# Kernel tuning notes

Measured on AMD Instinct MI355X. Metric: run time of the kernel, lower is better.

Reference implementation:

```python
import jax, jax.numpy as jnp
import numpy as np


def setup_inputs() -> dict:
    key = jax.random.key(0)
    k1, k2 = jax.random.split(key)
    B, C, H = 1024, 1000, 512  # batch, classes, hidden
    y = jax.random.normal(k1, (B, C), dtype=jnp.float32)
    w = jax.random.normal(k2, (C, H), dtype=jnp.float32)
    epsilon = jnp.ones((), dtype=jnp.float32)
    lipschitz = jnp.ones((), dtype=jnp.float32)
    return {"y": y, "w": w, "epsilon": epsilon, "lipschitz": lipschitz}


def reference(y, w, epsilon, lipschitz):
    # y: [B, C] logits; w: [C, H] final-layer weight
    kW = lipschitz * w.T                      # [H, C]
    j = jnp.argmax(y, axis=1)                 # [B]
    y_j = jnp.max(y, axis=1, keepdims=True)   # [B, 1]
    kW_j = kW.T[j]                            # [B, H] gather of argmax column
    kW_ij = kW_j[:, :, None] - kW[None]       # [B, H, C] broadcast difference
    sq = jnp.sum(kW_ij * kW_ij, axis=1)       # [B, C]
    # safe sqrt (value identical; avoids NaN grad at the exact-zero j column)
    K_ij = jnp.where(sq > 0, jnp.sqrt(jnp.where(sq > 0, sq, 1.0)), 0.0)
    y_bot_i = y + epsilon * K_ij              # [B, C]
    y_bot_i = jnp.where(y == y_j, -jnp.inf, y_bot_i)
    y_bot = jnp.max(y_bot_i, axis=1, keepdims=True)  # [B, 1]
    return jnp.concatenate([y, y_bot], axis=1)       # [B, C+1]
```

## Files before the change

### kernel.cpp

```cpp
#include <hip/hip_runtime.h>
#include <math.h>

#define B_SZ 1024
#define C_SZ 1000
#define H_SZ 512


typedef __attribute__((ext_vector_type(8))) short bf16x8;
typedef __attribute__((ext_vector_type(4))) float f32x4;

#define KC 128
#define RS 136

__device__ __forceinline__ uint4 pack8(float4 a, float4 b) {
    unsigned e[8] = {__float_as_uint(a.x), __float_as_uint(a.y),
                     __float_as_uint(a.z), __float_as_uint(a.w),
                     __float_as_uint(b.x), __float_as_uint(b.y),
                     __float_as_uint(b.z), __float_as_uint(b.w)};
    unsigned short h[8];
#pragma unroll
    for (int i = 0; i < 8; ++i) {
        unsigned v = e[i];
        v += 0x7fffu + ((v >> 16) & 1u);
        h[i] = (unsigned short)(v >> 16);
    }
    uint4 p;
    p.x = (unsigned)h[0] | ((unsigned)h[1] << 16);
    p.y = (unsigned)h[2] | ((unsigned)h[3] << 16);
    p.z = (unsigned)h[4] | ((unsigned)h[5] << 16);
    p.w = (unsigned)h[6] | ((unsigned)h[7] << 16);
    return p;
}

__device__ __forceinline__ float sumsq8(float4 a, float4 b) {
    return a.x * a.x + a.y * a.y + a.z * a.z + a.w * a.w +
           b.x * b.x + b.y * b.y + b.z * b.z + b.w * b.w;
}

__global__ __launch_bounds__(256) void k_main(
    const float* __restrict__ y, const float* __restrict__ w,
    const float* __restrict__ eps_p, const float* __restrict__ lip_p,
    float* __restrict__ part) {
    __shared__ __align__(16) short As[16 * RS];
    __shared__ __align__(16) short Bs[64 * RS];
    __shared__ int sjv[16];
    __shared__ float sym[16];
    __shared__ float snj[16];
    __shared__ float snc[64];
    __shared__ float wred[4][16];

    const int t = threadIdx.x;
    const int wv = t >> 6, lane = t & 63;
    const int col = lane & 15, quad = lane >> 4;
    const int bx = blockIdx.x, by = blockIdx.y;
    const int b0 = by * 16, c0 = bx * 64;

    {
        const int lr = t >> 4, seg = t & 15;
        const float* yrow = y + (b0 + lr) * C_SZ;
        float best = -INFINITY;
        int bidx = 0x7fffffff;
#pragma unroll
        for (int i = 0; i < 16; ++i) {
            const int idx = seg + i * 16;
            if (idx < 250) {
                float4 v = *(const float4*)(yrow + idx * 4);
                float e[4] = {v.x, v.y, v.z, v.w};
#pragma unroll
                for (int j = 0; j < 4; ++j) {
                    if (e[j] > best) { best = e[j]; bidx = idx * 4 + j; }
                }
            }
        }
#pragma unroll
        for (int off = 8; off; off >>= 1) {
            float ov = __shfl_xor(best, off, 64);
            int oi = __shfl_xor(bidx, off, 64);
            if (ov > best || (ov == best && oi < bidx)) { best = ov; bidx = oi; }
        }
        if (seg == 0) { sjv[lr] = bidx; sym[lr] = best; }
    }
    __syncthreads();

    const int arow = t >> 4;
    const int aseg = t & 15;
    const float* ag = w + sjv[arow] * H_SZ + aseg * 8;
    int brow_[4];
    const float* bg[4];
#pragma unroll
    for (int p = 0; p < 4; ++p) {
        const int idx = p * 256 + t;
        brow_[p] = idx >> 4;
        int cr = c0 + brow_[p];
        if (cr > C_SZ - 1) cr = C_SZ - 1;
        bg[p] = w + cr * H_SZ + aseg * 8;
    }

    float4 pa0 = *(const float4*)ag;
    float4 pa1 = *(const float4*)(ag + 4);
    float4 pb0[4], pb1[4];
#pragma unroll
    for (int p = 0; p < 4; ++p) {
        pb0[p] = *(const float4*)bg[p];
        pb1[p] = *(const float4*)(bg[p] + 4);
    }

    const short* ard = &As[col * RS + quad * 8];
    const short* brd = &Bs[(wv * 16 + col) * RS + quad * 8];

    f32x4 acc = {0.f, 0.f, 0.f, 0.f};
    float na = 0.f;
    float nb[4] = {0.f, 0.f, 0.f, 0.f};

    for (int ch = 0; ch < 4; ++ch) {
        na += sumsq8(pa0, pa1);
        *(uint4*)&As[arow * RS + aseg * 8] = pack8(pa0, pa1);
#pragma unroll
        for (int p = 0; p < 4; ++p) {
            nb[p] += sumsq8(pb0[p], pb1[p]);
            *(uint4*)&Bs[brow_[p] * RS + aseg * 8] = pack8(pb0[p], pb1[p]);
        }
        __syncthreads();
        if (ch < 3) {
            const int go = (ch + 1) * KC;
            pa0 = *(const float4*)(ag + go);
            pa1 = *(const float4*)(ag + go + 4);
#pragma unroll
            for (int p = 0; p < 4; ++p) {
                pb0[p] = *(const float4*)(bg[p] + go);
                pb1[p] = *(const float4*)(bg[p] + go + 4);
            }
        }
#pragma unroll
        for (int ks = 0; ks < 4; ++ks) {
            bf16x8 af = *(const bf16x8*)(ard + ks * 32);
            bf16x8 bf = *(const bf16x8*)(brd + ks * 32);
            acc = __builtin_amdgcn_mfma_f32_16x16x32_bf16(af, bf, acc, 0, 0, 0);
        }
        __syncthreads();
    }

#pragma unroll
    for (int off = 1; off < 16; off <<= 1) na += __shfl_xor(na, off, 64);
#pragma unroll
    for (int p = 0; p < 4; ++p)
#pragma unroll
        for (int off = 1; off < 16; off <<= 1)
            nb[p] += __shfl_xor(nb[p], off, 64);
    if (aseg == 0) {
        snj[arow] = na;
#pragma unroll
        for (int p = 0; p < 4; ++p) snc[brow_[p]] = nb[p];
    }
    __syncthreads();

    const float eps = *eps_p;
    const float L = *lip_p;
    const float L2 = L * L;
    const int cc = c0 + wv * 16 + col;
    const float nc = snc[wv * 16 + col];
    float rmax[4];
#pragma unroll
    for (int i = 0; i < 4; ++i) {
        const int br = quad * 4 + i;
        const int b = b0 + br;
        float cand = -INFINITY;
        if (cc < C_SZ) {
            const float yv = y[b * C_SZ + cc];
            const float sq = L2 * (snj[br] + nc - 2.0f * acc[i]);
            const float K = sq > 0.f ? sqrtf(sq) : 0.f;
            cand = (yv == sym[br]) ? -INFINITY : yv + eps * K;
        }
        rmax[i] = cand;
    }
#pragma unroll
    for (int off = 8; off; off >>= 1)
#pragma unroll
        for (int i = 0; i < 4; ++i)
            rmax[i] = fmaxf(rmax[i], __shfl_xor(rmax[i], off, 64));
    if (col == 0) {
#pragma unroll
        for (int i = 0; i < 4; ++i) wred[wv][quad * 4 + i] = rmax[i];
    }
    __syncthreads();
    if (t < 16) {
        float m = fmaxf(fmaxf(wred[0][t], wred[1][t]),
                        fmaxf(wred[2][t], wred[3][t]));
        __hip_atomic_store(&part[bx * B_SZ + b0 + t], m, __ATOMIC_RELAXED,
                           __HIP_MEMORY_SCOPE_AGENT);
    }
}

__global__ __launch_bounds__(256) void k_final(const float* __restrict__ y,
                                               float* __restrict__ part,
                                               float* __restrict__ out) {
    const int t = threadIdx.x;
    const int wv = t >> 6, lane = t & 63;
    const int b = blockIdx.x * 4 + wv;
    const float* yrow = y + b * C_SZ;
    float* orow = out + b * (C_SZ + 1);
#pragma unroll
    for (int i = 0; i < 4; ++i) {
        const int idx = i * 64 + lane;
        if (idx < 250)
            *(float4*)(orow + idx * 4) = *(const float4*)(yrow + idx * 4);
    }
    float m = -INFINITY;
    if (lane < 16)
        m = __hip_atomic_load(&part[lane * B_SZ + b], __ATOMIC_RELAXED,
                              __HIP_MEMORY_SCOPE_AGENT);
#pragma unroll
    for (int off = 8; off; off >>= 1) m = fmaxf(m, __shfl_xor(m, off, 64));
    if (lane == 0) orow[C_SZ] = m;
}

extern "C" void kernel_launch(void* const* d_in, const int* in_sizes, int n_in,
                              void* d_out, int out_size, void* d_ws,
                              size_t ws_size, hipStream_t stream) {
    const float* y = (const float*)d_in[0];
    const float* w = (const float*)d_in[1];
    const float* eps = (const float*)d_in[2];
    const float* lip = (const float*)d_in[3];
    float* out = (float*)d_out;
    float* part = (float*)d_ws;

    k_main<<<dim3(16, 64), 256, 0, stream>>>(y, w, eps, lip, part);
    k_final<<<B_SZ / 4, 256, 0, stream>>>(y, part, out);
}
```

Before: 82.80 us.

## Enlarge row tile to 64x64 with four MFMA accumulators per wave

Each block now covers 64 batch rows instead of 16, and each wave computes a 16x64 output strip with four accumulators while reusing one A fragment across four B fragments. Grid drops from 1024 to 256 blocks, so the class-side weights are loaded and converted far less often. The register prefetch pipeline is removed: each chunk is now loaded synchronously by two threads per row, and the final cross-wave reduction is replaced by direct per-wave stores. The risks are exposed load latency without prefetch, fewer blocks to fill the CUs, and a longer serial argmax (63 iterations per thread).

```diff
diff --git a/kernel.cpp b/kernel.cpp
--- a/kernel.cpp
+++ b/kernel.cpp
@@ -41,28 +41,27 @@
     const float* __restrict__ y, const float* __restrict__ w,
     const float* __restrict__ eps_p, const float* __restrict__ lip_p,
     float* __restrict__ part) {
-    __shared__ __align__(16) short As[16 * RS];
+    __shared__ __align__(16) short As[64 * RS];
     __shared__ __align__(16) short Bs[64 * RS];
-    __shared__ int sjv[16];
-    __shared__ float sym[16];
-    __shared__ float snj[16];
+    __shared__ int sjv[64];
+    __shared__ float sym[64];
+    __shared__ float snj[64];
     __shared__ float snc[64];
-    __shared__ float wred[4][16];
 
     const int t = threadIdx.x;
     const int wv = t >> 6, lane = t & 63;
     const int col = lane & 15, quad = lane >> 4;
     const int bx = blockIdx.x, by = blockIdx.y;
-    const int b0 = by * 16, c0 = bx * 64;
+    const int b0 = by * 64, c0 = bx * 64;
 
     {
-        const int lr = t >> 4, seg = t & 15;
+        const int lr = t >> 2, seg = t & 3;
         const float* yrow = y + (b0 + lr) * C_SZ;
         float best = -INFINITY;
         int bidx = 0x7fffffff;
 #pragma unroll
-        for (int i = 0; i < 16; ++i) {
-            const int idx = seg + i * 16;
+        for (int i = 0; i < 63; ++i) {
+            const int idx = i * 4 + seg;
             if (idx < 250) {
                 float4 v = *(const float4*)(yrow + idx * 4);
                 float e[4] = {v.x, v.y, v.z, v.w};
@@ -73,7 +72,7 @@
             }
         }
 #pragma unroll
-        for (int off = 8; off; off >>= 1) {
+        for (int off = 1; off < 4; off <<= 1) {
             float ov = __shfl_xor(best, off, 64);
             int oi = __shfl_xor(bidx, off, 64);
             if (ov > best || (ov == best && oi < bidx)) { best = ov; bidx = oi; }
@@ -82,96 +81,81 @@
     }
     __syncthreads();
 
-    const int arow = t >> 4;
-    const int aseg = t & 15;
-    const float* ag = w + sjv[arow] * H_SZ + aseg * 8;
-    int brow_[4];
-    const float* bg[4];
-#pragma unroll
-    for (int p = 0; p < 4; ++p) {
-        const int idx = p * 256 + t;
-        brow_[p] = idx >> 4;
-        int cr = c0 + brow_[p];
-        if (cr > C_SZ - 1) cr = C_SZ - 1;
-        bg[p] = w + cr * H_SZ + aseg * 8;
-    }
-
-    float4 pa0 = *(const float4*)ag;
-    float4 pa1 = *(const float4*)(ag + 4);
-    float4 pb0[4], pb1[4];
-#pragma unroll
-    for (int p = 0; p < 4; ++p) {
-        pb0[p] = *(const float4*)bg[p];
-        pb1[p] = *(const float4*)(bg[p] + 4);
-    }
-
-    const short* ard = &As[col * RS + quad * 8];
-    const short* brd = &Bs[(wv * 16 + col) * RS + quad * 8];
-
-    f32x4 acc = {0.f, 0.f, 0.f, 0.f};
-    float na = 0.f;
-    float nb[4] = {0.f, 0.f, 0.f, 0.f};
+    const int srow = t >> 1;
+    const int shalf = t & 1;
+    const bool isA = srow < 64;
+    const int lrow = isA ? srow : srow - 64;
+    int grow;
+    if (isA) {
+        grow = sjv[lrow];
+    } else {
+        grow = c0 + lrow;
+        if (grow > C_SZ - 1) grow = C_SZ - 1;
+    }
+    const float* gsrc = w + grow * H_SZ + shalf * 64;
+    short* ldst = (isA ? &As[lrow * RS] : &Bs[lrow * RS]) + shalf * 64;
+
+    const short* ard = &As[(wv * 16 + col) * RS + quad * 8];
+    const short* brd = &Bs[col * RS + quad * 8];
+
+    f32x4 acc[4] = {{0.f, 0.f, 0.f, 0.f},
+                    {0.f, 0.f, 0.f, 0.f},
+                    {0.f, 0.f, 0.f, 0.f},
+                    {0.f, 0.f, 0.f, 0.f}};
+    float nacc = 0.f;
 
     for (int ch = 0; ch < 4; ++ch) {
-        na += sumsq8(pa0, pa1);
-        *(uint4*)&As[arow * RS + aseg * 8] = pack8(pa0, pa1);
-#pragma unroll
-        for (int p = 0; p < 4; ++p) {
-            nb[p] += sumsq8(pb0[p], pb1[p]);
-            *(uint4*)&Bs[brow_[p] * RS + aseg * 8] = pack8(pb0[p], pb1[p]);
+#pragma unroll
+        for (int j = 0; j < 8; ++j) {
+            float4 a = *(const float4*)(gsrc + ch * KC + j * 8);
+            float4 b = *(const float4*)(gsrc + ch * KC + j * 8 + 4);
+            nacc += sumsq8(a, b);
+            *(uint4*)(ldst + j * 8) = pack8(a, b);
         }
         __syncthreads();
-        if (ch < 3) {
-            const int go = (ch + 1) * KC;
-            pa0 = *(const float4*)(ag + go);
-            pa1 = *(const float4*)(ag + go + 4);
-#pragma unroll
-            for (int p = 0; p < 4; ++p) {
-                pb0[p] = *(const float4*)(bg[p] + go);
-                pb1[p] = *(const float4*)(bg[p] + go + 4);
-            }
-        }
 #pragma unroll
         for (int ks = 0; ks < 4; ++ks) {
             bf16x8 af = *(const bf16x8*)(ard + ks * 32);
-            bf16x8 bf = *(const bf16x8*)(brd + ks * 32);
-            acc = __builtin_amdgcn_mfma_f32_16x16x32_bf16(af, bf, acc, 0, 0, 0);
+#pragma unroll
+            for (int ct = 0; ct < 4; ++ct) {
+                bf16x8 bf = *(const bf16x8*)(brd + ct * 16 * RS + ks * 32);
+                acc[ct] = __builtin_amdgcn_mfma_f32_16x16x32_bf16(af, bf,
+                                                                  acc[ct], 0, 0, 0);
+            }
         }
         __syncthreads();
     }
 
-#pragma unroll
-    for (int off = 1; off < 16; off <<= 1) na += __shfl_xor(na, off, 64);
-#pragma unroll
-    for (int p = 0; p < 4; ++p)
-#pragma unroll
-        for (int off = 1; off < 16; off <<= 1)
-            nb[p] += __shfl_xor(nb[p], off, 64);
-    if (aseg == 0) {
-        snj[arow] = na;
-#pragma unroll
-        for (int p = 0; p < 4; ++p) snc[brow_[p]] = nb[p];
+    nacc += __shfl_xor(nacc, 1, 64);
+    if (shalf == 0) {
+        if (isA) snj[lrow] = nacc;
+        else snc[lrow] = nacc;
     }
     __syncthreads();
 
     const float eps = *eps_p;
     const float L = *lip_p;
     const float L2 = L * L;
-    const int cc = c0 + wv * 16 + col;
-    const float nc = snc[wv * 16 + col];
     float rmax[4];
 #pragma unroll
     for (int i = 0; i < 4; ++i) {
-        const int br = quad * 4 + i;
+        const int br = wv * 16 + quad * 4 + i;
         const int b = b0 + br;
-        float cand = -INFINITY;
-        if (cc < C_SZ) {
-            const float yv = y[b * C_SZ + cc];
-            const float sq = L2 * (snj[br] + nc - 2.0f * acc[i]);
-            const float K = sq > 0.f ? sqrtf(sq) : 0.f;
-            cand = (yv == sym[br]) ? -INFINITY : yv + eps * K;
-        }
-        rmax[i] = cand;
+        const float nj = snj[br];
+        const float ym = sym[br];
+        float m = -INFINITY;
+#pragma unroll
+        for (int ct = 0; ct < 4; ++ct) {
+            const int cc = c0 + ct * 16 + col;
+            if (cc < C_SZ) {
+                const float yv = y[b * C_SZ + cc];
+                const float sq = L2 * (nj + snc[ct * 16 + col] - 2.0f * acc[ct][i]);
+                const float K = sq > 0.f ? sqrtf(sq) : 0.f;
+                const float cand = (yv == ym) ? -INFINITY : yv + eps * K;
+                m = fmaxf(m, cand);
+            }
+        }
+        rmax[i] = m;
     }
 #pragma unroll
     for (int off = 8; off; off >>= 1)
@@ -180,14 +164,10 @@
             rmax[i] = fmaxf(rmax[i], __shfl_xor(rmax[i], off, 64));
     if (col == 0) {
 #pragma unroll
-        for (int i = 0; i < 4; ++i) wred[wv][quad * 4 + i] = rmax[i];
-    }
-    __syncthreads();
-    if (t < 16) {
-        float m = fmaxf(fmaxf(wred[0][t], wred[1][t]),
-                        fmaxf(wred[2][t], wred[3][t]));
-        __hip_atomic_store(&part[bx * B_SZ + b0 + t], m, __ATOMIC_RELAXED,
-                           __HIP_MEMORY_SCOPE_AGENT);
+        for (int i = 0; i < 4; ++i)
+            __hip_atomic_store(&part[bx * B_SZ + b0 + wv * 16 + quad * 4 + i],
+                               rmax[i], __ATOMIC_RELAXED,
+                               __HIP_MEMORY_SCOPE_AGENT);
     }
 }
 
@@ -224,6 +204,6 @@
     float* out = (float*)d_out;
     float* part = (float*)d_ws;
 
-    k_main<<<dim3(16, 64), 256, 0, stream>>>(y, w, eps, lip, part);
+    k_main<<<dim3(16, 16), 256, 0, stream>>>(y, w, eps, lip, part);
     k_final<<<B_SZ / 4, 256, 0, stream>>>(y, part, out);
 }
```

Result: slower. 87.18 us (+5.3%).
